# Kernel optimization log

Hardware: AMD Instinct MI355X
Metric: run time of the kernel (lower is better)

Reference implementation:

```python
import jax, jax.numpy as jnp
import numpy as np

N_SITES = 1024
A_PER_SITE = 2
R_PER_ALLELE = 16
N_ALLELES = N_SITES * A_PER_SITE
N_READS = N_ALLELES * R_PER_ALLELE
C_IN, C, L = 16, 32, 150


def conv1d(x, w, stride=1, dilation=1, pad=2):
    return jax.lax.conv_general_dilated(
        x, w, (stride,), [(pad, pad)], rhs_dilation=(dilation,),
        dimension_numbers=('NCH', 'OIH', 'NCH'))


def reduce_slots(d, slots):
    # cumsum-diff segmented sum over dim 0, exactly as torch reduceSlots
    res = jnp.cumsum(d, axis=0)
    idx = jnp.cumsum(slots) - 1
    sel = res[idx]
    padded = jnp.concatenate([jnp.zeros_like(sel[:1]), sel[:-1]], axis=0)
    return sel - padded


def xattn(allele, site0, site1, wq, wk, wv, wo):
    # cross-attention: allele features query the two expanded site-feature streams
    q = jnp.einsum('oc,ncl->nol', wq, allele)
    kv = jnp.concatenate([site0, site1], axis=-1)  # [Na, C, 2*L']
    k = jnp.einsum('oc,ncl->nol', wk, kv)
    v = jnp.einsum('oc,ncl->nol', wv, kv)
    scores = jnp.einsum('ncl,ncm->nlm', q, k) / np.float32(np.sqrt(C))
    ctx = jnp.einsum('nlm,ncm->ncl', jax.nn.softmax(scores, axis=-1), v)
    return jnp.mean(allele + ctx, axis=-1) @ wo.T  # [Na, 2]


def setup_inputs():
    ks = jax.random.split(jax.random.key(0), 24)
    w = lambda i, shape: jax.random.normal(ks[i], shape, jnp.float32) * 0.05
    return {
        'tensors0': jax.random.normal(ks[0], (N_READS, C_IN, L), jnp.float32),
        'tensors1': jax.random.normal(ks[1], (N_READS, C_IN, L), jnp.float32),
        'conv0_w': w(2, (C, C_IN, 5)), 'conv1_w': w(3, (C, C_IN, 5)),
        'comp0_w': w(4, (C, C, 3)), 'comp1_w': w(5, (C, C, 3)), 'comp2_w': w(6, (C, C, 3)),
        'xq0': w(7, (C, C)), 'xk0': w(8, (C, C)), 'xv0': w(9, (C, C)), 'xo0': w(10, (2, C)),
        'xq1': w(11, (C, C)), 'xk1': w(12, (C, C)), 'xv1': w(13, (C, C)), 'xo1': w(14, (2, C)),
        'xq2': w(15, (C, C)), 'xk2': w(16, (C, C)), 'xv2': w(17, (C, C)), 'xo2': w(18, (2, C)),
        'comb_w': w(19, (C, 2 * C)), 'meta_w': w(20, (3, 2 * C)), 'meta_b': w(21, (3,)),
        'num_alleles_per_site': jnp.full((N_SITES,), A_PER_SITE, jnp.int32),
        'num_reads0': jnp.full((N_ALLELES,), R_PER_ALLELE, jnp.int32),
        'num_reads1': jnp.full((N_ALLELES,), R_PER_ALLELE, jnp.int32),
    }


def reference(tensors0, tensors1, conv0_w, conv1_w, comp0_w, comp1_w, comp2_w,
              xq0, xk0, xv0, xo0, xq1, xk1, xv1, xo1, xq2, xk2, xv2, xo2,
              comb_w, meta_w, meta_b, num_alleles_per_site, num_reads0, num_reads1):
    compressor = lambda x, w: jax.nn.relu(conv1d(x, w, stride=2, dilation=2, pad=2))

    def compress_and_predict(red_allele, comp_w, xw):
        cfa = compressor(red_allele, comp_w)                       # [Na, C, L']
        rfs = reduce_slots(red_allele, num_alleles_per_site)       # [Ns, C, L]
        cfs0 = compressor(rfs, comp_w)                             # [Ns, C, L']
        exp0 = jnp.repeat(cfs0, num_alleles_per_site, axis=0, total_repeat_length=N_ALLELES)
        cfs1 = reduce_slots(cfa, num_alleles_per_site)             # [Ns, C, L']
        exp1 = jnp.repeat(cfs1, num_alleles_per_site, axis=0, total_repeat_length=N_ALLELES)
        return xattn(cfa, exp0, exp1, *xw), (cfs0, cfs1)

    rc0 = jax.nn.relu(conv1d(tensors0, conv0_w, pad=2))            # [Nr, C, L]
    red0 = reduce_slots(rc0, num_reads0)                           # [Na, C, L]
    e0, _ = compress_and_predict(red0, comp0_w, (xq0, xk0, xv0, xo0))

    rc1 = jax.nn.relu(conv1d(tensors1, conv1_w, pad=2))
    red1 = reduce_slots(rc1, num_reads1)
    e1, _ = compress_and_predict(red1, comp1_w, (xq1, xk1, xv1, xo1))

    red2 = jax.nn.relu(jnp.einsum('oc,ncl->nol', comb_w, jnp.concatenate([red0, red1], axis=1)))
    e2, (s0, s1) = compress_and_predict(red2, comp2_w, (xq2, xk2, xv2, xo2))

    meta_feat = jnp.mean(jnp.concatenate([s0, s1], axis=1), axis=-1)  # [Ns, 2C]
    meta = jax.nn.softmax(meta_feat @ meta_w.T + meta_b, axis=-1)     # [Ns, 3]
    return (jnp.stack([e0, e1, e2]), meta)
```

## Files before the change

kernel.cpp:

```cpp
#include <hip/hip_runtime.h>
#include <math.h>

#define NS 1024
#define NA 2048
#define CIN 16
#define CC 32
#define LL 150
#define LC 75

typedef __attribute__((ext_vector_type(8))) short short8;
typedef __attribute__((ext_vector_type(4))) float float4v;

__device__ __forceinline__ unsigned short f2bf(float f) {
  unsigned int u = __float_as_uint(f);
  unsigned int r = (u + 0x7FFFu + ((u >> 16) & 1u)) >> 16;
  return (unsigned short)r;
}

__device__ __forceinline__ unsigned int pkbf(float lo, float hi) {
  return (unsigned int)f2bf(lo) | ((unsigned int)f2bf(hi) << 16);
}

__global__ __launch_bounds__(256) void k_conv_sum_mfma(const float* __restrict__ x,
                                                       const float* __restrict__ w,
                                                       float* __restrict__ red) {
  __shared__ unsigned short xs[2][154 * 32];
  const int a = blockIdx.x;
  const int tid = threadIdx.x;
  const int lane = tid & 63;
  const int wv = tid >> 6;

  short8 afr[2][3];
  {
    const int mrow = lane & 15;
    const int h = lane >> 4;
    for (int mt = 0; mt < 2; ++mt) {
      const int c = mt * 16 + mrow;
      for (int s = 0; s < 3; ++s) {
        short8 f;
#pragma unroll
        for (int j = 0; j < 8; ++j) {
          int ic = 4 * h + (j >> 1);
          int tap = 2 * s + (j & 1);
          float wval = (tap < 5) ? w[c * 80 + ic * 5 + tap] : 0.f;
          f[j] = (short)f2bf(wval);
        }
        afr[mt][s] = f;
      }
    }
  }

  float4v sum[2][3];
#pragma unroll
  for (int mt = 0; mt < 2; ++mt)
#pragma unroll
    for (int nt = 0; nt < 3; ++nt) sum[mt][nt] = (float4v)(0.f);

  const int nbase = wv * 48;
  const int nrow = lane & 15;
  const int hh = lane >> 4;
  const float4v zf = (float4v)(0.f);

  auto stage = [&](int r, int buf) {
    const float* xr = x + (size_t)(a * 16 + r) * (CIN * LL);
    unsigned int* xb32 = (unsigned int*)xs[buf];
    for (int idx = tid; idx < 16 * 38; idx += 256) {
      const int ic = idx & 15;
      const int seg = idx >> 4;
      const int l0 = seg * 4;
      const float* row = xr + ic * LL;
      float v0, v1, v2, v3, v4;
      if (seg < 37) {
        float2 u = *(const float2*)(row + l0);
        float2 u2 = *(const float2*)(row + l0 + 2);
        v0 = u.x; v1 = u.y; v2 = u2.x; v3 = u2.y;
        v4 = row[l0 + 4];
      } else {
        float2 u = *(const float2*)(row + 148);
        v0 = u.x; v1 = u.y; v2 = 0.f; v3 = 0.f; v4 = 0.f;
      }
      const int hb = 4 * (ic >> 2) + (ic & 3);
      unsigned int* b32 = xb32 + 16 * (l0 + 2) + hb;
      b32[0]  = pkbf(v0, v1);
      b32[16] = pkbf(v1, v2);
      b32[32] = pkbf(v2, v3);
      b32[48] = pkbf(v3, v4);
    }
    if (tid < 32) {
      const int ic = tid & 15;
      const int which = tid >> 4;
      const int hb = 4 * (ic >> 2) + (ic & 3);
      xb32[16 * which + hb] = which ? pkbf(0.f, xr[ic * LL]) : 0u;
    }
  };

  stage(0, 0);
  __syncthreads();

  for (int r = 0; r < 16; ++r) {
    const int cur = r & 1;
    if (r + 1 < 16) stage(r + 1, cur ^ 1);

    float4v acc[2][3];
#pragma unroll
    for (int s = 0; s < 3; ++s) {
#pragma unroll
      for (int nt = 0; nt < 3; ++nt) {
        int p = nbase + nt * 16 + nrow + 2 * s;
        if (p >= 154) p -= 154;
        short8 bfrag = *(const short8*)&xs[cur][(4 * p + hh) * 8];
#pragma unroll
        for (int mt = 0; mt < 2; ++mt) {
          acc[mt][nt] = __builtin_amdgcn_mfma_f32_16x16x32_bf16(
              afr[mt][s], bfrag, (s == 0) ? zf : acc[mt][nt], 0, 0, 0);
        }
      }
    }
#pragma unroll
    for (int mt = 0; mt < 2; ++mt)
#pragma unroll
      for (int nt = 0; nt < 3; ++nt)
#pragma unroll
        for (int q = 0; q < 4; ++q) sum[mt][nt][q] += fmaxf(acc[mt][nt][q], 0.f);

    __syncthreads();
  }

  const int ccol = lane & 15;
  const int crow4 = (lane >> 4) * 4;
  for (int mt = 0; mt < 2; ++mt)
    for (int nt = 0; nt < 3; ++nt) {
      int l = nbase + nt * 16 + ccol;
      if (l < LL) {
#pragma unroll
        for (int q = 0; q < 4; ++q) {
          int c = mt * 16 + crow4 + q;
          red[(size_t)a * (CC * LL) + c * LL + l] = sum[mt][nt][q];
        }
      }
    }
}

__global__ __launch_bounds__(256) void k_comb(const float* __restrict__ red0,
                                              const float* __restrict__ red1,
                                              const float* __restrict__ cw,
                                              float* __restrict__ out) {
  __shared__ float ins[64][152];
  __shared__ float cwl[64][CC];
  const int a = blockIdx.x;
  const int tid = threadIdx.x;

  for (int i = tid; i < 64 * CC; i += 256) {
    int c = i & 31; int c2 = i >> 5;
    cwl[c2][c] = cw[c * 64 + c2];
  }
  for (int i = tid; i < CC * LL; i += 256) {
    int c2 = i / LL; int l = i - c2 * LL;
    ins[c2][l] = red0[(size_t)a * (CC * LL) + i];
    ins[32 + c2][l] = red1[(size_t)a * (CC * LL) + i];
  }
  __syncthreads();

  const int c = tid & 31;
  const int lg = tid >> 5;
  const int l0 = lg * 19;
  const int nl = (LL - l0 < 19) ? (LL - l0) : 19;
  float v[19];
#pragma unroll
  for (int j = 0; j < 19; ++j) v[j] = 0.f;
  for (int c2 = 0; c2 < 64; ++c2) {
    float wv = cwl[c2][c];
#pragma unroll
    for (int j = 0; j < 19; ++j) v[j] += wv * ins[c2][l0 + j];
  }
  float* o = out + (size_t)a * (CC * LL) + c * LL + l0;
  for (int j = 0; j < nl; ++j) o[j] = fmaxf(v[j], 0.f);
}

__global__ __launch_bounds__(256) void k_compress2(const float* __restrict__ src,
                                                   const float* __restrict__ w,
                                                   float* __restrict__ cfa,
                                                   float* __restrict__ cfs) {
  __shared__ float ins0[CC][164];
  __shared__ float ins1[CC][164];
  __shared__ float ws[CC][3][CC];
  const int sfull = blockIdx.x;
  const int tid = threadIdx.x;

  for (int i = tid; i < CC * 3 * CC; i += 256) {
    int c = i & 31; int kk = i >> 5; int ic = kk / 3; int t = kk - ic * 3;
    ws[ic][t][c] = w[c * (CC * 3) + ic * 3 + t];
  }
  if (tid < CC) {
    ins0[tid][0] = 0.f; ins0[tid][1] = 0.f; ins0[tid][152] = 0.f; ins0[tid][153] = 0.f;
    ins1[tid][0] = 0.f; ins1[tid][1] = 0.f; ins1[tid][152] = 0.f; ins1[tid][153] = 0.f;
  }
  {
    const float* s0 = src + (size_t)(2 * sfull) * (CC * LL);
    const float* s1 = s0 + CC * LL;
    for (int i = tid; i < CC * LL; i += 256) {
      int ic = i / LL; int l = i - ic * LL;
      ins0[ic][l + 2] = s0[i];
      ins1[ic][l + 2] = s1[i];
    }
  }
  __syncthreads();

  const int c = tid & 31;
  const int jg = tid >> 5;
  const int j0 = jg * 10;
  const int nj = (LC - j0 < 10) ? (LC - j0) : 10;
  float v0[10], v1[10];
#pragma unroll
  for (int j = 0; j < 10; ++j) { v0[j] = 0.f; v1[j] = 0.f; }
  for (int ic = 0; ic < CC; ++ic) {
    float w0 = ws[ic][0][c], w1 = ws[ic][1][c], w2 = ws[ic][2][c];
    float xa[12], xb[12];
#pragma unroll
    for (int i = 0; i < 12; ++i) {
      xa[i] = ins0[ic][2 * j0 + 2 * i];
      xb[i] = ins1[ic][2 * j0 + 2 * i];
    }
#pragma unroll
    for (int j = 0; j < 10; ++j) {
      v0[j] += w0 * xa[j] + w1 * xa[j + 1] + w2 * xa[j + 2];
      v1[j] += w0 * xb[j] + w1 * xb[j + 1] + w2 * xb[j + 2];
    }
  }
  float* oa0 = cfa + (size_t)(2 * sfull) * (CC * LC) + c * LC + j0;
  float* oa1 = oa0 + CC * LC;
  float* os  = cfs + (size_t)sfull * (CC * LC) + c * LC + j0;
  for (int j = 0; j < nj; ++j) {
    float a0 = v0[j], a1 = v1[j];
    oa0[j] = fmaxf(a0, 0.f);
    oa1[j] = fmaxf(a1, 0.f);
    os[j]  = fmaxf(a0 + a1, 0.f);
  }
}

#define BKV   0
#define BW    4800
#define BQT   8064
#define BCF   10464
#define BKB   10464
#define BVB   15328
#define BROWP 0
#define BPART 6080
#define BMS   6336
#define ARENA 20320

__global__ __launch_bounds__(256) void k_attn(const float* __restrict__ cfa,
                                              const float* __restrict__ cfs0,
                                              const float* __restrict__ wq,
                                              const float* __restrict__ wk,
                                              const float* __restrict__ wv,
                                              const float* __restrict__ wo,
                                              float* __restrict__ eout) {
  __shared__ float ar[ARENA];
  const int a = blockIdx.x;
  const int s = a >> 1;
  const int tid = threadIdx.x;
  const int g = tid >> 5;
  const int t = tid & 31;

  for (int i = tid; i < CC * CC; i += 256) {
    int o = i >> 5, ii = i & 31;
    ar[BW + ii * 33 + o]        = wq[i];
    ar[BW + 1056 + ii * 33 + o] = wk[i];
    ar[BW + 2112 + ii * 33 + o] = wv[i];
  }
  {
    const float* sg = cfs0 + (size_t)s * (CC * LC);
    const float* a0 = cfa + (size_t)(2 * s) * (CC * LC);
    const float* a1 = a0 + CC * LC;
    const int sel = a & 1;
    for (int i = tid; i < CC * LC; i += 256) {
      int c = i / 75, l = i - c * 75;
      float v0 = a0[i], v1 = a1[i];
      ar[BKV + c * 150 + l]      = sg[i];
      ar[BKV + c * 150 + 75 + l] = v0 + v1;
      ar[BCF + c * 77 + l]       = sel ? v1 : v0;
    }
  }
  __syncthreads();

  float cfp = 0.f;
  {
    float wqc[32];
#pragma unroll
    for (int ii = 0; ii < 32; ++ii) wqc[ii] = ar[BW + ii * 33 + t];
    for (int row = g; row < 75; row += 8) {
      float acc = 0.f;
#pragma unroll
      for (int ii = 0; ii < 32; ++ii) acc += wqc[ii] * ar[BCF + ii * 77 + row];
      ar[BQT + row * 32 + t] = acc;
      cfp += ar[BCF + t * 77 + row];
    }
  }
  __syncthreads();

  {
    float wkc[32], wvc[32];
#pragma unroll
    for (int ii = 0; ii < 32; ++ii) {
      wkc[ii] = ar[BW + 1056 + ii * 33 + t];
      wvc[ii] = ar[BW + 2112 + ii * 33 + t];
    }
    for (int idx = tid; idx < CC * LL; idx += 256) {
      int o = idx & 31, m = idx >> 5;
      float ka = 0.f, va = 0.f;
#pragma unroll
      for (int ii = 0; ii < 32; ++ii) {
        float x = ar[BKV + ii * 150 + m];
        ka += wkc[ii] * x;
        va += wvc[ii] * x;
      }
      ar[BKB + o * 152 + m] = ka;
      ar[BVB + o * 156 + m] = va;
    }
    if (tid < 64) ar[BVB + (tid >> 1) * 156 + 150 + (tid & 1)] = 0.f;
  }
  __syncthreads();

  float ms = 0.f;
  const int rbase = BROWP + g * 760;
  const float scale = 0.17677669529663687f;
#pragma unroll 1
  for (int cc = 0; cc < 2; ++cc) {
    const int ch = g + 8 * cc;
    if (ch >= 15) break;
    const int r0 = ch * 5;

    float2 acc[5][3];
#pragma unroll
    for (int i = 0; i < 5; ++i)
#pragma unroll
      for (int u = 0; u < 3; ++u) acc[i][u] = make_float2(0.f, 0.f);

#pragma unroll 1
    for (int c2 = 0; c2 < 32; c2 += 2) {
      float2 q01[5];
#pragma unroll
      for (int i = 0; i < 5; ++i) q01[i] = *(const float2*)&ar[BQT + (r0 + i) * 32 + c2];
      const int cb0 = BKB + c2 * 152 + 2 * t;
      const int cb1 = cb0 + 152;
      float2 ka0 = *(const float2*)&ar[cb0];
      float2 ka1 = *(const float2*)&ar[cb0 + 64];
      float2 ka2 = *(const float2*)&ar[cb0 + 128];
      float2 kb0 = *(const float2*)&ar[cb1];
      float2 kb1 = *(const float2*)&ar[cb1 + 64];
      float2 kb2 = *(const float2*)&ar[cb1 + 128];
#pragma unroll
      for (int i = 0; i < 5; ++i) {
        acc[i][0].x += q01[i].x * ka0.x + q01[i].y * kb0.x;
        acc[i][0].y += q01[i].x * ka0.y + q01[i].y * kb0.y;
        acc[i][1].x += q01[i].x * ka1.x + q01[i].y * kb1.x;
        acc[i][1].y += q01[i].x * ka1.y + q01[i].y * kb1.y;
        acc[i][2].x += q01[i].x * ka2.x + q01[i].y * kb2.x;
        acc[i][2].y += q01[i].x * ka2.y + q01[i].y * kb2.y;
      }
    }

    float inv[5];
#pragma unroll
    for (int i = 0; i < 5; ++i) {
      float s0x = acc[i][0].x * scale, s0y = acc[i][0].y * scale;
      float s1x = acc[i][1].x * scale, s1y = acc[i][1].y * scale;
      float s2x = acc[i][2].x * scale, s2y = acc[i][2].y * scale;
      if (t >= 11) { s2x = -1e30f; s2y = -1e30f; }
      float mx = fmaxf(fmaxf(fmaxf(s0x, s0y), fmaxf(s1x, s1y)), fmaxf(s2x, s2y));
#pragma unroll
      for (int off = 16; off > 0; off >>= 1) mx = fmaxf(mx, __shfl_xor(mx, off, 32));
      float p0x = __expf(s0x - mx), p0y = __expf(s0y - mx);
      float p1x = __expf(s1x - mx), p1y = __expf(s1y - mx);
      float p2x = __expf(s2x - mx), p2y = __expf(s2y - mx);
      float ss = p0x + p0y + p1x + p1y + p2x + p2y;
#pragma unroll
      for (int off = 16; off > 0; off >>= 1) ss += __shfl_xor(ss, off, 32);
      inv[i] = 1.f / ss;
      const int rb = rbase + i * 152 + 2 * t;
      *(float2*)&ar[rb]      = make_float2(p0x, p0y);
      *(float2*)&ar[rb + 64] = make_float2(p1x, p1y);
      if (t <= 11) *(float2*)&ar[rb + 128] = make_float2(p2x, p2y);
    }

    float pv[5] = {0.f, 0.f, 0.f, 0.f, 0.f};
    for (int mq = 0; mq < 38; ++mq) {
      float4 vv = *(const float4*)&ar[BVB + t * 156 + 4 * mq];
#pragma unroll
      for (int i = 0; i < 5; ++i) {
        float4 pp = *(const float4*)&ar[rbase + i * 152 + 4 * mq];
        pv[i] += pp.x * vv.x + pp.y * vv.y + pp.z * vv.z + pp.w * vv.w;
      }
    }
#pragma unroll
    for (int i = 0; i < 5; ++i) ms += pv[i] * inv[i];
  }

  ar[BPART + g * 32 + t] = cfp + ms;
  __syncthreads();

  if (tid < 32) {
    float tot = 0.f;
#pragma unroll
    for (int gg = 0; gg < 8; ++gg) tot += ar[BPART + gg * 32 + tid];
    ar[BMS + tid] = tot * (1.f / 75.f);
  }
  __syncthreads();
  if (tid < 2) {
    float e = 0.f;
#pragma unroll
    for (int c2 = 0; c2 < CC; ++c2) e += wo[tid * CC + c2] * ar[BMS + c2];
    eout[a * 2 + tid] = e;
  }
}

__global__ __launch_bounds__(64) void k_meta(const float* __restrict__ cfs0,
                                             const float* __restrict__ cfa2,
                                             const float* __restrict__ mw,
                                             const float* __restrict__ mb,
                                             float* __restrict__ mout) {
  __shared__ float feat[64];
  __shared__ float lgt[3];
  const int s = blockIdx.x;
  const int tid = threadIdx.x;
  float f = 0.f;
  if (tid < 32) {
    const float* p = cfs0 + (size_t)s * (CC * LC) + tid * LC;
    for (int l = 0; l < LC; ++l) f += p[l];
  } else {
    const float* p0 = cfa2 + (size_t)(2 * s) * (CC * LC) + (tid - 32) * LC;
    const float* p1 = cfa2 + (size_t)(2 * s + 1) * (CC * LC) + (tid - 32) * LC;
    for (int l = 0; l < LC; ++l) f += p0[l] + p1[l];
  }
  feat[tid] = f * (1.f / 75.f);
  __syncthreads();
  if (tid < 3) {
    float acc2 = mb[tid];
    for (int c2 = 0; c2 < 64; ++c2) acc2 += mw[tid * 64 + c2] * feat[c2];
    lgt[tid] = acc2;
  }
  __syncthreads();
  if (tid < 3) {
    float mx = fmaxf(lgt[0], fmaxf(lgt[1], lgt[2]));
    float e0 = __expf(lgt[0] - mx), e1 = __expf(lgt[1] - mx), e2 = __expf(lgt[2] - mx);
    mout[s * 3 + tid] = __expf(lgt[tid] - mx) / (e0 + e1 + e2);
  }
}

extern "C" void kernel_launch(void* const* d_in, const int* in_sizes, int n_in,
                              void* d_out, int out_size, void* d_ws, size_t ws_size,
                              hipStream_t stream) {
  const float* t0      = (const float*)d_in[0];
  const float* t1      = (const float*)d_in[1];
  const float* conv0_w = (const float*)d_in[2];
  const float* conv1_w = (const float*)d_in[3];
  const float* comp0_w = (const float*)d_in[4];
  const float* comp1_w = (const float*)d_in[5];
  const float* comp2_w = (const float*)d_in[6];
  const float* xq0 = (const float*)d_in[7];
  const float* xk0 = (const float*)d_in[8];
  const float* xv0 = (const float*)d_in[9];
  const float* xo0 = (const float*)d_in[10];
  const float* xq1 = (const float*)d_in[11];
  const float* xk1 = (const float*)d_in[12];
  const float* xv1 = (const float*)d_in[13];
  const float* xo1 = (const float*)d_in[14];
  const float* xq2 = (const float*)d_in[15];
  const float* xk2 = (const float*)d_in[16];
  const float* xv2 = (const float*)d_in[17];
  const float* xo2 = (const float*)d_in[18];
  const float* comb_w = (const float*)d_in[19];
  const float* meta_w = (const float*)d_in[20];
  const float* meta_b = (const float*)d_in[21];

  float* wsf  = (float*)d_ws;
  float* red0 = wsf;
  float* red1 = red0 + (size_t)NA * CC * LL;
  float* cfa  = red1 + (size_t)NA * CC * LL;
  float* cfs0 = cfa + (size_t)NA * CC * LC;
  float* out  = (float*)d_out;

  k_conv_sum_mfma<<<NA, 256, 0, stream>>>(t0, conv0_w, red0);
  k_conv_sum_mfma<<<NA, 256, 0, stream>>>(t1, conv1_w, red1);

  k_compress2<<<NS, 256, 0, stream>>>(red0, comp0_w, cfa, cfs0);
  k_attn<<<NA, 256, 0, stream>>>(cfa, cfs0, xq0, xk0, xv0, xo0, out + 0);

  k_compress2<<<NS, 256, 0, stream>>>(red1, comp1_w, cfa, cfs0);
  k_attn<<<NA, 256, 0, stream>>>(cfa, cfs0, xq1, xk1, xv1, xo1, out + 2 * NA);

  k_comb<<<NA, 256, 0, stream>>>(red0, red1, comb_w, red0);
  k_compress2<<<NS, 256, 0, stream>>>(red0, comp2_w, cfa, cfs0);
  k_attn<<<NA, 256, 0, stream>>>(cfa, cfs0, xq2, xk2, xv2, xo2, out + 4 * NA);

  k_meta<<<NS, 64, 0, stream>>>(cfs0, cfa, meta_w, meta_b, out + 6 * NA);
}
```

Before: 1.480 ms.

## Process both alleles of a site in one attention block to share K/V

The attention kernel now launches one block per site instead of one per allele. The K and V projections of the shared site key/value stream are computed once and reused for both alleles; only the query projection is recomputed for the second allele, which reads its features straight from global memory. This halves the redundant K/V projection work and staging, at the cost of half as many blocks and a longer serial chain per block.

```diff
diff --git a/kernel.cpp b/kernel.cpp
--- a/kernel.cpp
+++ b/kernel.cpp
@@ -239,92 +239,22 @@
 }
 
 #define BKV   0
-#define BW    4800
-#define BQT   8064
-#define BCF   10464
-#define BKB   10464
-#define BVB   15328
+#define BWK   4800
+#define BWV   5856
+#define BWQ   6912
+#define BQT   7968
+#define BCF   10368
+#define BKB   10368
+#define BVB   15232
 #define BROWP 0
 #define BPART 6080
-#define BMS   6336
-#define ARENA 20320
-
-__global__ __launch_bounds__(256) void k_attn(const float* __restrict__ cfa,
-                                              const float* __restrict__ cfs0,
-                                              const float* __restrict__ wq,
-                                              const float* __restrict__ wk,
-                                              const float* __restrict__ wv,
-                                              const float* __restrict__ wo,
-                                              float* __restrict__ eout) {
-  __shared__ float ar[ARENA];
-  const int a = blockIdx.x;
-  const int s = a >> 1;
-  const int tid = threadIdx.x;
-  const int g = tid >> 5;
-  const int t = tid & 31;
-
-  for (int i = tid; i < CC * CC; i += 256) {
-    int o = i >> 5, ii = i & 31;
-    ar[BW + ii * 33 + o]        = wq[i];
-    ar[BW + 1056 + ii * 33 + o] = wk[i];
-    ar[BW + 2112 + ii * 33 + o] = wv[i];
-  }
-  {
-    const float* sg = cfs0 + (size_t)s * (CC * LC);
-    const float* a0 = cfa + (size_t)(2 * s) * (CC * LC);
-    const float* a1 = a0 + CC * LC;
-    const int sel = a & 1;
-    for (int i = tid; i < CC * LC; i += 256) {
-      int c = i / 75, l = i - c * 75;
-      float v0 = a0[i], v1 = a1[i];
-      ar[BKV + c * 150 + l]      = sg[i];
-      ar[BKV + c * 150 + 75 + l] = v0 + v1;
-      ar[BCF + c * 77 + l]       = sel ? v1 : v0;
-    }
-  }
-  __syncthreads();
-
-  float cfp = 0.f;
-  {
-    float wqc[32];
-#pragma unroll
-    for (int ii = 0; ii < 32; ++ii) wqc[ii] = ar[BW + ii * 33 + t];
-    for (int row = g; row < 75; row += 8) {
-      float acc = 0.f;
-#pragma unroll
-      for (int ii = 0; ii < 32; ++ii) acc += wqc[ii] * ar[BCF + ii * 77 + row];
-      ar[BQT + row * 32 + t] = acc;
-      cfp += ar[BCF + t * 77 + row];
-    }
-  }
-  __syncthreads();
-
-  {
-    float wkc[32], wvc[32];
-#pragma unroll
-    for (int ii = 0; ii < 32; ++ii) {
-      wkc[ii] = ar[BW + 1056 + ii * 33 + t];
-      wvc[ii] = ar[BW + 2112 + ii * 33 + t];
-    }
-    for (int idx = tid; idx < CC * LL; idx += 256) {
-      int o = idx & 31, m = idx >> 5;
-      float ka = 0.f, va = 0.f;
-#pragma unroll
-      for (int ii = 0; ii < 32; ++ii) {
-        float x = ar[BKV + ii * 150 + m];
-        ka += wkc[ii] * x;
-        va += wvc[ii] * x;
-      }
-      ar[BKB + o * 152 + m] = ka;
-      ar[BVB + o * 156 + m] = va;
-    }
-    if (tid < 64) ar[BVB + (tid >> 1) * 156 + 150 + (tid & 1)] = 0.f;
-  }
-  __syncthreads();
-
-  float ms = 0.f;
+#define BMS   6592
+#define ARENA 20224
+
+__device__ __forceinline__ void attn_phase_d(float* __restrict__ ar, int g, int t,
+                                             float& ms) {
+  const float scale = 0.17677669529663687f;
   const int rbase = BROWP + g * 760;
-  const float scale = 0.17677669529663687f;
 #pragma unroll 1
   for (int cc = 0; cc < 2; ++cc) {
     const int ch = g + 8 * cc;
@@ -396,22 +326,120 @@
 #pragma unroll
     for (int i = 0; i < 5; ++i) ms += pv[i] * inv[i];
   }
-
-  ar[BPART + g * 32 + t] = cfp + ms;
-  __syncthreads();
-
-  if (tid < 32) {
+}
+
+__global__ __launch_bounds__(256) void k_attn(const float* __restrict__ cfa,
+                                              const float* __restrict__ cfs0,
+                                              const float* __restrict__ wq,
+                                              const float* __restrict__ wk,
+                                              const float* __restrict__ wv,
+                                              const float* __restrict__ wo,
+                                              float* __restrict__ eout) {
+  __shared__ float ar[ARENA];
+  const int s = blockIdx.x;
+  const int tid = threadIdx.x;
+  const int g = tid >> 5;
+  const int t = tid & 31;
+
+  const float* a0g = cfa + (size_t)(2 * s) * (CC * LC);
+  const float* a1g = a0g + CC * LC;
+
+  for (int i = tid; i < CC * CC; i += 256) {
+    int o = i >> 5, ii = i & 31;
+    ar[BWQ + ii * 33 + o] = wq[i];
+    ar[BWK + ii * 33 + o] = wk[i];
+    ar[BWV + ii * 33 + o] = wv[i];
+  }
+  {
+    const float* sg = cfs0 + (size_t)s * (CC * LC);
+    for (int i = tid; i < CC * LC; i += 256) {
+      int c = i / 75, l = i - c * 75;
+      float v0 = a0g[i], v1 = a1g[i];
+      ar[BKV + c * 150 + l]      = sg[i];
+      ar[BKV + c * 150 + 75 + l] = v0 + v1;
+      ar[BCF + c * 77 + l]       = v0;
+    }
+  }
+  __syncthreads();
+
+  float cfp0 = 0.f;
+  {
+    float wqc[32];
+#pragma unroll
+    for (int ii = 0; ii < 32; ++ii) wqc[ii] = ar[BWQ + ii * 33 + t];
+    for (int row = g; row < 75; row += 8) {
+      float acc = 0.f;
+#pragma unroll
+      for (int ii = 0; ii < 32; ++ii) acc += wqc[ii] * ar[BCF + ii * 77 + row];
+      ar[BQT + row * 32 + t] = acc;
+      cfp0 += ar[BCF + t * 77 + row];
+    }
+  }
+  __syncthreads();
+
+  {
+    float wkc[32], wvc[32];
+#pragma unroll
+    for (int ii = 0; ii < 32; ++ii) {
+      wkc[ii] = ar[BWK + ii * 33 + t];
+      wvc[ii] = ar[BWV + ii * 33 + t];
+    }
+    for (int idx = tid; idx < CC * LL; idx += 256) {
+      int o = idx & 31, m = idx >> 5;
+      float ka = 0.f, va = 0.f;
+#pragma unroll
+      for (int ii = 0; ii < 32; ++ii) {
+        float x = ar[BKV + ii * 150 + m];
+        ka += wkc[ii] * x;
+        va += wvc[ii] * x;
+      }
+      ar[BKB + o * 152 + m] = ka;
+      ar[BVB + o * 156 + m] = va;
+    }
+    if (tid < 64) ar[BVB + (tid >> 1) * 156 + 150 + (tid & 1)] = 0.f;
+  }
+  __syncthreads();
+
+  float ms0 = 0.f;
+  attn_phase_d(ar, g, t, ms0);
+  __syncthreads();
+
+  float cfp1 = 0.f;
+  {
+    float wqc[32];
+#pragma unroll
+    for (int ii = 0; ii < 32; ++ii) wqc[ii] = ar[BWQ + ii * 33 + t];
+    for (int row = g; row < 75; row += 8) {
+      float acc = 0.f;
+#pragma unroll
+      for (int ii = 0; ii < 32; ++ii) acc += wqc[ii] * a1g[ii * 75 + row];
+      ar[BQT + row * 32 + t] = acc;
+      cfp1 += a1g[t * 75 + row];
+    }
+  }
+  __syncthreads();
+
+  float ms1 = 0.f;
+  attn_phase_d(ar, g, t, ms1);
+
+  ar[BPART + g * 32 + t]       = cfp0 + ms0;
+  ar[BPART + 256 + g * 32 + t] = cfp1 + ms1;
+  __syncthreads();
+
+  if (tid < 64) {
+    int al = tid >> 5, tt = tid & 31;
     float tot = 0.f;
 #pragma unroll
-    for (int gg = 0; gg < 8; ++gg) tot += ar[BPART + gg * 32 + tid];
-    ar[BMS + tid] = tot * (1.f / 75.f);
-  }
-  __syncthreads();
-  if (tid < 2) {
+    for (int gg = 0; gg < 8; ++gg) tot += ar[BPART + al * 256 + gg * 32 + tt];
+    ar[BMS + al * 32 + tt] = tot * (1.f / 75.f);
+  }
+  __syncthreads();
+  if (tid < 4) {
+    int al = tid >> 1, o2 = tid & 1;
     float e = 0.f;
 #pragma unroll
-    for (int c2 = 0; c2 < CC; ++c2) e += wo[tid * CC + c2] * ar[BMS + c2];
-    eout[a * 2 + tid] = e;
+    for (int c2 = 0; c2 < CC; ++c2) e += wo[o2 * CC + c2] * ar[BMS + al * 32 + c2];
+    eout[s * 4 + tid] = e;
   }
 }
 
@@ -485,14 +513,14 @@
   k_conv_sum_mfma<<<NA, 256, 0, stream>>>(t1, conv1_w, red1);
 
   k_compress2<<<NS, 256, 0, stream>>>(red0, comp0_w, cfa, cfs0);
-  k_attn<<<NA, 256, 0, stream>>>(cfa, cfs0, xq0, xk0, xv0, xo0, out + 0);
+  k_attn<<<NS, 256, 0, stream>>>(cfa, cfs0, xq0, xk0, xv0, xo0, out + 0);
 
   k_compress2<<<NS, 256, 0, stream>>>(red1, comp1_w, cfa, cfs0);
-  k_attn<<<NA, 256, 0, stream>>>(cfa, cfs0, xq1, xk1, xv1, xo1, out + 2 * NA);
+  k_attn<<<NS, 256, 0, stream>>>(cfa, cfs0, xq1, xk1, xv1, xo1, out + 2 * NA);
 
   k_comb<<<NA, 256, 0, stream>>>(red0, red1, comb_w, red0);
   k_compress2<<<NS, 256, 0, stream>>>(red0, comp2_w, cfa, cfs0);
-  k_attn<<<NA, 256, 0, stream>>>(cfa, cfs0, xq2, xk2, xv2, xo2, out + 4 * NA);
+  k_attn<<<NS, 256, 0, stream>>>(cfa, cfs0, xq2, xk2, xv2, xo2, out + 4 * NA);
 
   k_meta<<<NS, 64, 0, stream>>>(cfs0, cfa, meta_w, meta_b, out + 6 * NA);
 }
```

Measured after the change: 1.398 ms. 5.5% less time.
